# Kernel optimization log

Hardware: AMD Instinct MI355X
Metric: run time of the kernel (lower is better)

The kernel has to match this reference:

```python
import jax, jax.numpy as jnp
import numpy as np

B, S, D, H, F = 8, 1024, 768, 12, 3072
DH = D // H
C_QUAD = 5.0
LN_EPS = 1e-5


def layer_norm(x, g, b):
    mu = jnp.mean(x, axis=-1, keepdims=True)
    var = jnp.mean(jnp.square(x - mu), axis=-1, keepdims=True)
    return (x - mu) * jax.lax.rsqrt(var + LN_EPS) * g + b


def setup_inputs() -> dict:
    key = jax.random.key(0)
    ks = jax.random.split(key, 8)
    s_in = 1.0 / np.sqrt(D)
    s_ff = 1.0 / np.sqrt(F)
    return {
        "x": jax.random.normal(ks[0], (B, S, D), jnp.float32),
        "wqkv": jax.random.normal(ks[1], (D, 3 * D), jnp.float32) * s_in,
        "bqkv": jnp.zeros((3 * D,), jnp.float32),
        "wo": jax.random.normal(ks[2], (D, D), jnp.float32) * s_in,
        "bo": jnp.zeros((D,), jnp.float32),
        "ln1_g": jnp.ones((D,), jnp.float32),
        "ln1_b": jnp.zeros((D,), jnp.float32),
        "w1": jax.random.normal(ks[3], (D, F), jnp.float32) * s_in,
        "b1": jnp.zeros((F,), jnp.float32),
        "w2": jax.random.normal(ks[4], (F, D), jnp.float32) * s_ff,
        "b2": jnp.zeros((D,), jnp.float32),
        "ln2_g": jnp.ones((D,), jnp.float32),
        "ln2_b": jnp.zeros((D,), jnp.float32),
    }


def quad2(scores):
    # Quad2 custom 'softmax': (s + c)^2 normalized by row sum
    s2 = jnp.square(scores + C_QUAD)
    return s2 / jnp.sum(s2, axis=-1, keepdims=True)


def reference(x, wqkv, bqkv, wo, bo, ln1_g, ln1_b, w1, b1, w2, b2, ln2_g, ln2_b):
    # --- pre-norm multi-head attention with Quad2 score normalization ---
    h = layer_norm(x, ln1_g, ln1_b)
    qkv = h @ wqkv + bqkv                              # [B,S,3D]
    q, k, v = jnp.split(qkv, 3, axis=-1)
    q = q.reshape(B, S, H, DH).transpose(0, 2, 1, 3)   # [B,H,S,Dh]
    k = k.reshape(B, S, H, DH).transpose(0, 2, 1, 3)
    v = v.reshape(B, S, H, DH).transpose(0, 2, 1, 3)
    scale = 1.0 / np.sqrt(DH)
    scores = jnp.einsum("bhqd,bhkd->bhqk", q, k) * scale
    attn = quad2(scores)                               # [B,H,S,S]
    ctx = jnp.einsum("bhqk,bhkd->bhqd", attn, v)
    ctx = ctx.transpose(0, 2, 1, 3).reshape(B, S, D)
    x = x + ctx @ wo + bo
    # --- pre-norm FFN ---
    h = layer_norm(x, ln2_g, ln2_b)
    h = jax.nn.gelu(h @ w1 + b1)
    x = x + h @ w2 + b2
    return x
```

## Files before the change

### kernel.cpp

```cpp
#include <hip/hip_runtime.h>
#include <hip/hip_bf16.h>

constexpr int B_ = 8;
constexpr int S_ = 1024;
constexpr int D_ = 768;
constexpr int H_ = 12;
constexpr int F_ = 3072;
constexpr int DH_ = 64;
constexpr int M_ = B_ * S_;
constexpr int PSZ = B_ * S_ * D_;

typedef __bf16 bf16x8 __attribute__((ext_vector_type(8)));
typedef float f32x4 __attribute__((ext_vector_type(4)));
typedef short s16x8 __attribute__((ext_vector_type(8)));
typedef short s16x4 __attribute__((ext_vector_type(4)));

__device__ __forceinline__ void gload_lds16(const __bf16* g, __bf16* l) {
    __builtin_amdgcn_global_load_lds(
        (const __attribute__((address_space(1))) void*)g,
        (__attribute__((address_space(3))) void*)l,
        16, 0, 0);
}

__device__ __forceinline__ float fast_gelu(float x) {
    float x3 = x * x * x;
    float z = 0.7978845608028654f * x + 0.035677408136300125f * x3;
    float e = __builtin_amdgcn_exp2f(-2.8853900817779268f * z);
    return x * __builtin_amdgcn_rcpf(1.0f + e);
}

__global__ __launch_bounds__(256) void transpose_cvt(const float* __restrict__ in,
                                                     __bf16* __restrict__ out,
                                                     int K, int N) {
    __shared__ float t[32][33];
    int tx = threadIdx.x, ty = threadIdx.y;
    int n0 = blockIdx.x * 32, k0 = blockIdx.y * 32;
#pragma unroll
    for (int i = 0; i < 4; ++i)
        t[ty + i * 8][tx] = in[(size_t)(k0 + ty + i * 8) * N + n0 + tx];
    __syncthreads();
#pragma unroll
    for (int i = 0; i < 4; ++i)
        out[(size_t)(n0 + ty + i * 8) * K + k0 + tx] = (__bf16)t[tx][ty + i * 8];
}

__global__ __launch_bounds__(256) void ln_kernel(const float* __restrict__ x,
                                                 const float* __restrict__ g,
                                                 const float* __restrict__ bb,
                                                 __bf16* __restrict__ out) {
    int row = blockIdx.x;
    const float* xr = x + (size_t)row * D_;
    int tid = threadIdx.x;
    float v[3];
    float s = 0.f, s2 = 0.f;
#pragma unroll
    for (int j = 0; j < 3; ++j) {
        v[j] = xr[tid + j * 256];
        s += v[j];
        s2 += v[j] * v[j];
    }
#pragma unroll
    for (int o = 32; o >= 1; o >>= 1) {
        s += __shfl_xor(s, o, 64);
        s2 += __shfl_xor(s2, o, 64);
    }
    __shared__ float red[8];
    int wid = tid >> 6, lane = tid & 63;
    if (lane == 0) { red[wid] = s; red[4 + wid] = s2; }
    __syncthreads();
    s = red[0] + red[1] + red[2] + red[3];
    s2 = red[4] + red[5] + red[6] + red[7];
    float mu = s * (1.0f / D_);
    float var = s2 * (1.0f / D_) - mu * mu;
    float rs = rsqrtf(var + 1e-5f);
    __bf16* orow = out + (size_t)row * D_;
#pragma unroll
    for (int j = 0; j < 3; ++j) {
        int i = tid + j * 256;
        orow[i] = (__bf16)((v[j] - mu) * rs * g[i] + bb[i]);
    }
}

template <int EPI>
__device__ __forceinline__ void gemm4_body(const __bf16* __restrict__ A,
                                           const __bf16* __restrict__ Bt,
                                           const float* __restrict__ bias,
                                           const float* __restrict__ res,
                                           float* __restrict__ outf,
                                           __bf16* __restrict__ outb,
                                           int M, int N, int K) {
    __shared__ __bf16 lds[2][16384];

    const int tid = threadIdx.x;
    const int lane = tid & 63, wid = tid >> 6;
    const int wm = wid >> 1, wn = wid & 1;
    const int gx = gridDim.x;
    const int nwg = gx * gridDim.y;
    int flat = blockIdx.y * gx + blockIdx.x;
    flat = (flat & 7) * (nwg >> 3) + (flat >> 3);
    const int bm = (flat / gx) * 128, bn = (flat % gx) * 128;
    const int l15 = lane & 15, l4 = lane >> 4;
    f32x4 acc[4][4] = {};

    const int r8 = tid >> 3;
    const int swc = ((tid & 7) ^ (r8 & 7)) * 8;
    const __bf16* ga = A + (size_t)(bm + r8) * K + swc;
    const __bf16* gb = Bt + (size_t)(bn + r8) * K + swc;
    const int NT = K / 64;

    auto stage = [&](int t, int s) {
        const int kt = t * 64;
        __bf16* base = &lds[s][0] + tid * 8;
#pragma unroll
        for (int j = 0; j < 4; ++j)
            gload_lds16(ga + kt + (size_t)j * 32 * K, base + j * 2048);
#pragma unroll
        for (int j = 0; j < 4; ++j)
            gload_lds16(gb + kt + (size_t)j * 32 * K, base + 8192 + j * 2048);
    };

    stage(0, 0);
    for (int t = 0; t < NT; ++t) {
        if (t + 1 < NT) {
            stage(t + 1, (t + 1) & 1);
            asm volatile("s_waitcnt vmcnt(8)" ::: "memory");
        } else {
            asm volatile("s_waitcnt vmcnt(0)" ::: "memory");
        }
        asm volatile("s_barrier" ::: "memory");

        const __bf16* sA = &lds[t & 1][0];
        const __bf16* sB = sA + 8192;
        const int swr = (l15 & 7) * 8;
        bf16x8 a[4][2], b[4][2];
#pragma unroll
        for (int mf = 0; mf < 4; ++mf) {
            int row = wm * 64 + mf * 16 + l15;
#pragma unroll
            for (int ks = 0; ks < 2; ++ks)
                a[mf][ks] = *(const bf16x8*)&sA[row * 64 + ((ks * 32 + l4 * 8) ^ swr)];
        }
#pragma unroll
        for (int nf = 0; nf < 4; ++nf) {
            int row = wn * 64 + nf * 16 + l15;
#pragma unroll
            for (int ks = 0; ks < 2; ++ks)
                b[nf][ks] = *(const bf16x8*)&sB[row * 64 + ((ks * 32 + l4 * 8) ^ swr)];
        }
        asm volatile("s_waitcnt lgkmcnt(0)" ::: "memory");
        asm volatile("s_barrier" ::: "memory");
        __builtin_amdgcn_sched_barrier(0);

        __builtin_amdgcn_s_setprio(1);
#pragma unroll
        for (int ks = 0; ks < 2; ++ks)
#pragma unroll
            for (int mf = 0; mf < 4; ++mf)
#pragma unroll
                for (int nf = 0; nf < 4; ++nf)
                    acc[mf][nf] = __builtin_amdgcn_mfma_f32_16x16x32_bf16(
                        a[mf][ks], b[nf][ks], acc[mf][nf], 0, 0, 0);
        __builtin_amdgcn_s_setprio(0);
    }

    if constexpr (EPI == 0) {
#pragma unroll
        for (int nf = 0; nf < 4; ++nf) {
            int n = bn + wn * 64 + nf * 16 + l15;
            int part = n / 768;
            int n7 = n - part * 768;
            float bv = bias[n];
            size_t obase = (size_t)part * PSZ + (size_t)(n7 >> 6) * (S_ * DH_) + (n7 & 63);
#pragma unroll
            for (int mf = 0; mf < 4; ++mf) {
                int m0 = bm + wm * 64 + mf * 16 + l4 * 4;
                size_t rb = obase + (size_t)(m0 >> 10) * ((size_t)H_ * S_ * DH_) +
                            (size_t)(m0 & 1023) * DH_;
#pragma unroll
                for (int r = 0; r < 4; ++r)
                    outb[rb + (size_t)r * DH_] = (__bf16)(acc[mf][nf][r] + bv);
            }
        }
    } else {
#pragma unroll
        for (int mf = 0; mf < 4; ++mf) {
#pragma unroll
            for (int nf = 0; nf < 4; ++nf) {
#pragma unroll
                for (int r = 0; r < 4; ++r) {
                    int m = bm + wm * 64 + mf * 16 + l4 * 4 + r;
                    int n = bn + wn * 64 + nf * 16 + l15;
                    float val = acc[mf][nf][r] + bias[n];
                    if constexpr (EPI == 1) {
                        outf[(size_t)m * N + n] = val + res[(size_t)m * N + n];
                    } else {
                        outb[(size_t)m * N + n] = (__bf16)fast_gelu(val);
                    }
                }
            }
        }
    }
}

template <int EPI>
__device__ __forceinline__ void gemmk_body(const __bf16* __restrict__ A,
                                           const __bf16* __restrict__ Bt,
                                           const float* __restrict__ bias,
                                           const float* __restrict__ res,
                                           float* __restrict__ outf,
                                           __bf16* __restrict__ outb,
                                           int M, int N, int K) {
    __shared__ __bf16 lds[2][16384];

    const int tid = threadIdx.x;
    const int lane = tid & 63, wid = tid >> 6;
    const int wm = wid >> 2, wn = wid & 3;
    const int gx = gridDim.x;
    const int nwg = gx * gridDim.y;
    int flat = blockIdx.y * gx + blockIdx.x;
    flat = (flat & 7) * (nwg >> 3) + (flat >> 3);
    const int bm = (flat / gx) * 128, bn = (flat % gx) * 128;
    const int l15 = lane & 15, l4 = lane >> 4;
    f32x4 acc[4][2] = {};

    const int r8 = tid >> 3;
    const int swc = ((tid & 7) ^ (r8 & 7)) * 8;
    const __bf16* ga = A + (size_t)(bm + r8) * K + swc;
    const __bf16* gb = Bt + (size_t)(bn + r8) * K + swc;
    const int NT = K / 64;

    auto stage = [&](int t, int s) {
        const int kt = t * 64;
        __bf16* base = &lds[s][0] + tid * 8;
        gload_lds16(ga + kt, base);
        gload_lds16(ga + kt + (size_t)64 * K, base + 4096);
        gload_lds16(gb + kt, base + 8192);
        gload_lds16(gb + kt + (size_t)64 * K, base + 12288);
    };

    stage(0, 0);
    for (int t = 0; t < NT; ++t) {
        if (t + 1 < NT) {
            stage(t + 1, (t + 1) & 1);
            asm volatile("s_waitcnt vmcnt(4)" ::: "memory");
        } else {
            asm volatile("s_waitcnt vmcnt(0)" ::: "memory");
        }
        asm volatile("s_barrier" ::: "memory");

        const __bf16* sA = &lds[t & 1][0];
        const __bf16* sB = sA + 8192;
        const int swr = (l15 & 7) * 8;
        bf16x8 a[4][2], b[2][2];
#pragma unroll
        for (int mf = 0; mf < 4; ++mf) {
            int row = wm * 64 + mf * 16 + l15;
#pragma unroll
            for (int ks = 0; ks < 2; ++ks)
                a[mf][ks] = *(const bf16x8*)&sA[row * 64 + ((ks * 32 + l4 * 8) ^ swr)];
        }
#pragma unroll
        for (int nf = 0; nf < 2; ++nf) {
            int row = wn * 32 + nf * 16 + l15;
#pragma unroll
            for (int ks = 0; ks < 2; ++ks)
                b[nf][ks] = *(const bf16x8*)&sB[row * 64 + ((ks * 32 + l4 * 8) ^ swr)];
        }
        asm volatile("s_waitcnt lgkmcnt(0)" ::: "memory");
        asm volatile("s_barrier" ::: "memory");
        __builtin_amdgcn_sched_barrier(0);

        __builtin_amdgcn_s_setprio(1);
#pragma unroll
        for (int ks = 0; ks < 2; ++ks)
#pragma unroll
            for (int mf = 0; mf < 4; ++mf)
#pragma unroll
                for (int nf = 0; nf < 2; ++nf)
                    acc[mf][nf] = __builtin_amdgcn_mfma_f32_16x16x32_bf16(
                        a[mf][ks], b[nf][ks], acc[mf][nf], 0, 0, 0);
        __builtin_amdgcn_s_setprio(0);
    }

#pragma unroll
    for (int mf = 0; mf < 4; ++mf) {
#pragma unroll
        for (int nf = 0; nf < 2; ++nf) {
#pragma unroll
            for (int r = 0; r < 4; ++r) {
                int m = bm + wm * 64 + mf * 16 + l4 * 4 + r;
                int n = bn + wn * 32 + nf * 16 + l15;
                float val = acc[mf][nf][r] + bias[n];
                if constexpr (EPI == 1) {
                    outf[(size_t)m * N + n] = val + res[(size_t)m * N + n];
                } else {
                    outb[(size_t)m * N + n] = (__bf16)fast_gelu(val);
                }
            }
        }
    }
    (void)outf;
}

__global__ __launch_bounds__(256) void g_qkv(const __bf16* A, const __bf16* Bt,
                                             const float* bias, __bf16* outb) {
    gemm4_body<0>(A, Bt, bias, nullptr, nullptr, outb, M_, 3 * D_, D_);
}
__global__ __launch_bounds__(256) void g_proj(const __bf16* A, const __bf16* Bt,
                                              const float* bias, const float* res,
                                              float* outf) {
    gemm4_body<1>(A, Bt, bias, res, outf, nullptr, M_, D_, D_);
}
__global__ __launch_bounds__(512) void g_ffn1(const __bf16* A, const __bf16* Bt,
                                              const float* bias, __bf16* outb) {
    gemmk_body<2>(A, Bt, bias, nullptr, nullptr, outb, M_, F_, D_);
}
__global__ __launch_bounds__(512) void g_ffn2(const __bf16* A, const __bf16* Bt,
                                              const float* bias, const float* res,
                                              float* outf) {
    gemmk_body<1>(A, Bt, bias, res, outf, nullptr, M_, D_, F_);
}

__global__ __launch_bounds__(256) void attn_kernel(const __bf16* __restrict__ qg,
                                                   const __bf16* __restrict__ kg,
                                                   const __bf16* __restrict__ vg,
                                                   __bf16* __restrict__ ctx) {
    __shared__ __bf16 Ks[64][72];
    __shared__ __bf16 Vt[64][72];
    __shared__ __bf16 Pw[4][32][72];
    __shared__ float den_l[4][32];
    int tid = threadIdx.x, lane = tid & 63, wid = tid >> 6;
    int l15 = lane & 15, l4 = lane >> 4;
    int idx = blockIdx.x;
    int xcd = idx & 7;
    int c = idx >> 3;
    int bh = xcd * 12 + (c >> 3);
    int qt = c & 7;
    int q0 = qt * 128;
    const __bf16* qbase = qg + (size_t)bh * S_ * DH_;
    const __bf16* kbase = kg + (size_t)bh * S_ * DH_;
    const __bf16* vbase = vg + (size_t)bh * S_ * DH_;

    int wq0 = q0 + wid * 32;
    bf16x8 qf[2][2];
#pragma unroll
    for (int qi = 0; qi < 2; ++qi)
#pragma unroll
        for (int ks = 0; ks < 2; ++ks)
            qf[qi][ks] = *(const bf16x8*)(qbase + (size_t)(wq0 + qi * 16 + l15) * DH_ +
                                          ks * 32 + l4 * 8);

    f32x4 oacc[2][4] = {};
    float den[2] = {0.f, 0.f};
    const float scale = 0.125f;

    for (int k0 = 0; k0 < S_; k0 += 64) {
        {
            int key = tid >> 2, dc = (tid & 3) * 16;
            *(s16x8*)&Ks[key][dc] =
                *(const s16x8*)(kbase + (size_t)(k0 + key) * DH_ + dc);
            *(s16x8*)&Ks[key][dc + 8] =
                *(const s16x8*)(kbase + (size_t)(k0 + key) * DH_ + dc + 8);
            int vkey = tid & 63, dg = (tid >> 6) * 16;
            s16x8 v0 = *(const s16x8*)(vbase + (size_t)(k0 + vkey) * DH_ + dg);
            s16x8 v1 = *(const s16x8*)(vbase + (size_t)(k0 + vkey) * DH_ + dg + 8);
#pragma unroll
            for (int e = 0; e < 8; ++e) {
                Vt[dg + e][vkey] = ((const __bf16*)&v0)[e];
                Vt[dg + 8 + e][vkey] = ((const __bf16*)&v1)[e];
            }
        }
        __syncthreads();

        bf16x8 kf[4][2];
#pragma unroll
        for (int kfi = 0; kfi < 4; ++kfi)
#pragma unroll
            for (int ks = 0; ks < 2; ++ks)
                kf[kfi][ks] = *(const bf16x8*)&Ks[kfi * 16 + l15][ks * 32 + l4 * 8];

#pragma unroll
        for (int qi = 0; qi < 2; ++qi) {
#pragma unroll
            for (int kfi = 0; kfi < 4; ++kfi) {
                f32x4 sa = {};
                sa = __builtin_amdgcn_mfma_f32_16x16x32_bf16(kf[kfi][0], qf[qi][0], sa, 0, 0, 0);
                sa = __builtin_amdgcn_mfma_f32_16x16x32_bf16(kf[kfi][1], qf[qi][1], sa, 0, 0, 0);
                __bf16 pk[4];
#pragma unroll
                for (int r = 0; r < 4; ++r) {
                    float p = sa[r] * scale + 5.0f;
                    p = p * p;
                    den[qi] += p;
                    pk[r] = (__bf16)p;
                }
                *(s16x4*)&Pw[wid][qi * 16 + l15][kfi * 16 + l4 * 4] =
                    *(const s16x4*)pk;
            }
        }

#pragma unroll
        for (int mf = 0; mf < 2; ++mf) {
#pragma unroll
            for (int ks = 0; ks < 2; ++ks) {
                bf16x8 pa = *(const bf16x8*)&Pw[wid][mf * 16 + l15][ks * 32 + l4 * 8];
#pragma unroll
                for (int nf = 0; nf < 4; ++nf) {
                    bf16x8 vb = *(const bf16x8*)&Vt[nf * 16 + l15][ks * 32 + l4 * 8];
                    oacc[mf][nf] = __builtin_amdgcn_mfma_f32_16x16x32_bf16(
                        pa, vb, oacc[mf][nf], 0, 0, 0);
                }
            }
        }
        __syncthreads();
    }

#pragma unroll
    for (int qi = 0; qi < 2; ++qi) {
        den[qi] += __shfl_xor(den[qi], 16, 64);
        den[qi] += __shfl_xor(den[qi], 32, 64);
    }
    if (lane < 16) {
        den_l[wid][lane] = den[0];
        den_l[wid][16 + lane] = den[1];
    }
    __syncthreads();

    int b_ = bh / H_, h_ = bh - b_ * H_;
#pragma unroll
    for (int mf = 0; mf < 2; ++mf)
#pragma unroll
        for (int nf = 0; nf < 4; ++nf) {
#pragma unroll
            for (int r = 0; r < 4; ++r) {
                int qrow = mf * 16 + l4 * 4 + r;
                int dcol = nf * 16 + l15;
                float val = oacc[mf][nf][r] *
                            __builtin_amdgcn_rcpf(den_l[wid][qrow]);
                int sI = q0 + wid * 32 + qrow;
                ctx[((size_t)b_ * S_ + sI) * D_ + h_ * DH_ + dcol] = (__bf16)val;
            }
        }
}

extern "C" void kernel_launch(void* const* d_in, const int* in_sizes, int n_in,
                              void* d_out, int out_size, void* d_ws, size_t ws_size,
                              hipStream_t stream) {
    const float* x    = (const float*)d_in[0];
    const float* wqkv = (const float*)d_in[1];
    const float* bqkv = (const float*)d_in[2];
    const float* wo   = (const float*)d_in[3];
    const float* bo   = (const float*)d_in[4];
    const float* ln1g = (const float*)d_in[5];
    const float* ln1b = (const float*)d_in[6];
    const float* w1   = (const float*)d_in[7];
    const float* b1   = (const float*)d_in[8];
    const float* w2   = (const float*)d_in[9];
    const float* b2   = (const float*)d_in[10];
    const float* ln2g = (const float*)d_in[11];
    const float* ln2b = (const float*)d_in[12];
    float* out = (float*)d_out;

    char* ws = (char*)d_ws;
    size_t off = 0;
    auto alloc = [&](size_t bytes) {
        void* p = ws + off;
        off += (bytes + 255) & ~(size_t)255;
        return p;
    };
    __bf16* wqkvT = (__bf16*)alloc((size_t)(3 * D_) * D_ * 2);
    __bf16* woT   = (__bf16*)alloc((size_t)D_ * D_ * 2);
    __bf16* w1T   = (__bf16*)alloc((size_t)F_ * D_ * 2);
    __bf16* w2T   = (__bf16*)alloc((size_t)D_ * F_ * 2);
    float*  X2    = (float*)alloc((size_t)M_ * D_ * 4);
    __bf16* Hb    = (__bf16*)alloc((size_t)M_ * D_ * 2);
    __bf16* Q3    = (__bf16*)alloc((size_t)4 * PSZ * 2);
    __bf16* Kb = Q3 + (size_t)PSZ;
    __bf16* Vb = Q3 + (size_t)2 * PSZ;
    __bf16* Cx = Q3 + (size_t)3 * PSZ;

    transpose_cvt<<<dim3((3 * D_) / 32, D_ / 32), dim3(32, 8), 0, stream>>>(wqkv, wqkvT, D_, 3 * D_);
    transpose_cvt<<<dim3(D_ / 32, D_ / 32), dim3(32, 8), 0, stream>>>(wo, woT, D_, D_);
    transpose_cvt<<<dim3(F_ / 32, D_ / 32), dim3(32, 8), 0, stream>>>(w1, w1T, D_, F_);
    transpose_cvt<<<dim3(D_ / 32, F_ / 32), dim3(32, 8), 0, stream>>>(w2, w2T, F_, D_);

    ln_kernel<<<M_, 256, 0, stream>>>(x, ln1g, ln1b, Hb);
    g_qkv<<<dim3((3 * D_) / 128, M_ / 128), 256, 0, stream>>>(Hb, wqkvT, bqkv, Q3);
    attn_kernel<<<B_ * H_ * (S_ / 128), 256, 0, stream>>>(Q3, Kb, Vb, Cx);
    g_proj<<<dim3(D_ / 128, M_ / 128), 256, 0, stream>>>(Cx, woT, bo, x, X2);
    ln_kernel<<<M_, 256, 0, stream>>>(X2, ln2g, ln2b, Hb);
    g_ffn1<<<dim3(F_ / 128, M_ / 128), 512, 0, stream>>>(Hb, w1T, b1, Q3);
    g_ffn2<<<dim3(D_ / 128, M_ / 128), 512, 0, stream>>>(Q3, w2T, b2, X2, out);
    (void)in_sizes; (void)n_in; (void)out_size; (void)ws_size;
}
```

Baseline: 226.1 us.

## Replace 512-thread FFN GEMM with 256-thread triple-buffered K32 kernel, simplify attention mapping

```diff
diff --git a/kernel.cpp b/kernel.cpp
--- a/kernel.cpp
+++ b/kernel.cpp
@@ -203,68 +203,62 @@
 }
 
 template <int EPI>
-__device__ __forceinline__ void gemmk_body(const __bf16* __restrict__ A,
-                                           const __bf16* __restrict__ Bt,
-                                           const float* __restrict__ bias,
-                                           const float* __restrict__ res,
-                                           float* __restrict__ outf,
-                                           __bf16* __restrict__ outb,
-                                           int M, int N, int K) {
-    __shared__ __bf16 lds[2][16384];
+__device__ __forceinline__ void gemm32_body(const __bf16* __restrict__ A,
+                                            const __bf16* __restrict__ Bt,
+                                            const float* __restrict__ bias,
+                                            const float* __restrict__ res,
+                                            float* __restrict__ outf,
+                                            __bf16* __restrict__ outb,
+                                            int M, int N, int K) {
+    __shared__ __bf16 lds[3][8192];
 
     const int tid = threadIdx.x;
     const int lane = tid & 63, wid = tid >> 6;
-    const int wm = wid >> 2, wn = wid & 3;
+    const int wm = wid >> 1, wn = wid & 1;
     const int gx = gridDim.x;
     const int nwg = gx * gridDim.y;
     int flat = blockIdx.y * gx + blockIdx.x;
     flat = (flat & 7) * (nwg >> 3) + (flat >> 3);
     const int bm = (flat / gx) * 128, bn = (flat % gx) * 128;
     const int l15 = lane & 15, l4 = lane >> 4;
-    f32x4 acc[4][2] = {};
-
-    const int r8 = tid >> 3;
-    const int swc = ((tid & 7) ^ (r8 & 7)) * 8;
+    f32x4 acc[4][4] = {};
+
+    const int r8 = tid >> 2;
+    const int cg = tid & 3;
+    const int swc = (cg ^ (r8 & 3)) * 8;
     const __bf16* ga = A + (size_t)(bm + r8) * K + swc;
     const __bf16* gb = Bt + (size_t)(bn + r8) * K + swc;
-    const int NT = K / 64;
+    const int NT = K / 32;
 
     auto stage = [&](int t, int s) {
-        const int kt = t * 64;
+        const int kt = t * 32;
         __bf16* base = &lds[s][0] + tid * 8;
         gload_lds16(ga + kt, base);
-        gload_lds16(ga + kt + (size_t)64 * K, base + 4096);
-        gload_lds16(gb + kt, base + 8192);
-        gload_lds16(gb + kt + (size_t)64 * K, base + 12288);
+        gload_lds16(ga + kt + (size_t)64 * K, base + 2048);
+        gload_lds16(gb + kt, base + 4096);
+        gload_lds16(gb + kt + (size_t)64 * K, base + 6144);
     };
 
     stage(0, 0);
+    stage(1, 1);
     for (int t = 0; t < NT; ++t) {
-        if (t + 1 < NT) {
-            stage(t + 1, (t + 1) & 1);
-            asm volatile("s_waitcnt vmcnt(4)" ::: "memory");
-        } else {
-            asm volatile("s_waitcnt vmcnt(0)" ::: "memory");
-        }
+        stage(t + 2 < NT ? t + 2 : NT - 1, (t + 2) % 3);
+        asm volatile("s_waitcnt vmcnt(8)" ::: "memory");
         asm volatile("s_barrier" ::: "memory");
 
-        const __bf16* sA = &lds[t & 1][0];
-        const __bf16* sB = sA + 8192;
-        const int swr = (l15 & 7) * 8;
-        bf16x8 a[4][2], b[2][2];
+        const __bf16* sA = &lds[t % 3][0];
+        const __bf16* sB = sA + 4096;
+        const int swr = (l15 & 3) * 8;
+        bf16x8 a[4], b[4];
 #pragma unroll
         for (int mf = 0; mf < 4; ++mf) {
             int row = wm * 64 + mf * 16 + l15;
-#pragma unroll
-            for (int ks = 0; ks < 2; ++ks)
-                a[mf][ks] = *(const bf16x8*)&sA[row * 64 + ((ks * 32 + l4 * 8) ^ swr)];
-        }
-#pragma unroll
-        for (int nf = 0; nf < 2; ++nf) {
-            int row = wn * 32 + nf * 16 + l15;
-#pragma unroll
-            for (int ks = 0; ks < 2; ++ks)
-                b[nf][ks] = *(const bf16x8*)&sB[row * 64 + ((ks * 32 + l4 * 8) ^ swr)];
+            a[mf] = *(const bf16x8*)&sA[row * 32 + ((l4 * 8) ^ swr)];
+        }
+#pragma unroll
+        for (int nf = 0; nf < 4; ++nf) {
+            int row = wn * 64 + nf * 16 + l15;
+            b[nf] = *(const bf16x8*)&sB[row * 32 + ((l4 * 8) ^ swr)];
         }
         asm volatile("s_waitcnt lgkmcnt(0)" ::: "memory");
         asm volatile("s_barrier" ::: "memory");
@@ -272,24 +266,22 @@
 
         __builtin_amdgcn_s_setprio(1);
 #pragma unroll
-        for (int ks = 0; ks < 2; ++ks)
-#pragma unroll
-            for (int mf = 0; mf < 4; ++mf)
-#pragma unroll
-                for (int nf = 0; nf < 2; ++nf)
-                    acc[mf][nf] = __builtin_amdgcn_mfma_f32_16x16x32_bf16(
-                        a[mf][ks], b[nf][ks], acc[mf][nf], 0, 0, 0);
+        for (int mf = 0; mf < 4; ++mf)
+#pragma unroll
+            for (int nf = 0; nf < 4; ++nf)
+                acc[mf][nf] = __builtin_amdgcn_mfma_f32_16x16x32_bf16(
+                    a[mf], b[nf], acc[mf][nf], 0, 0, 0);
         __builtin_amdgcn_s_setprio(0);
     }
 
 #pragma unroll
     for (int mf = 0; mf < 4; ++mf) {
 #pragma unroll
-        for (int nf = 0; nf < 2; ++nf) {
+        for (int nf = 0; nf < 4; ++nf) {
 #pragma unroll
             for (int r = 0; r < 4; ++r) {
                 int m = bm + wm * 64 + mf * 16 + l4 * 4 + r;
-                int n = bn + wn * 32 + nf * 16 + l15;
+                int n = bn + wn * 64 + nf * 16 + l15;
                 float val = acc[mf][nf][r] + bias[n];
                 if constexpr (EPI == 1) {
                     outf[(size_t)m * N + n] = val + res[(size_t)m * N + n];
@@ -311,14 +303,14 @@
                                               float* outf) {
     gemm4_body<1>(A, Bt, bias, res, outf, nullptr, M_, D_, D_);
 }
-__global__ __launch_bounds__(512) void g_ffn1(const __bf16* A, const __bf16* Bt,
+__global__ __launch_bounds__(256) void g_ffn1(const __bf16* A, const __bf16* Bt,
                                               const float* bias, __bf16* outb) {
-    gemmk_body<2>(A, Bt, bias, nullptr, nullptr, outb, M_, F_, D_);
-}
-__global__ __launch_bounds__(512) void g_ffn2(const __bf16* A, const __bf16* Bt,
+    gemm32_body<2>(A, Bt, bias, nullptr, nullptr, outb, M_, F_, D_);
+}
+__global__ __launch_bounds__(256) void g_ffn2(const __bf16* A, const __bf16* Bt,
                                               const float* bias, const float* res,
                                               float* outf) {
-    gemmk_body<1>(A, Bt, bias, res, outf, nullptr, M_, D_, F_);
+    gemm4_body<1>(A, Bt, bias, res, outf, nullptr, M_, D_, F_);
 }
 
 __global__ __launch_bounds__(256) void attn_kernel(const __bf16* __restrict__ qg,
@@ -331,11 +323,7 @@
     __shared__ float den_l[4][32];
     int tid = threadIdx.x, lane = tid & 63, wid = tid >> 6;
     int l15 = lane & 15, l4 = lane >> 4;
-    int idx = blockIdx.x;
-    int xcd = idx & 7;
-    int c = idx >> 3;
-    int bh = xcd * 12 + (c >> 3);
-    int qt = c & 7;
+    int bh = blockIdx.x >> 3, qt = blockIdx.x & 7;
     int q0 = qt * 128;
     const __bf16* qbase = qg + (size_t)bh * S_ * DH_;
     const __bf16* kbase = kg + (size_t)bh * S_ * DH_;
@@ -489,7 +477,7 @@
     attn_kernel<<<B_ * H_ * (S_ / 128), 256, 0, stream>>>(Q3, Kb, Vb, Cx);
     g_proj<<<dim3(D_ / 128, M_ / 128), 256, 0, stream>>>(Cx, woT, bo, x, X2);
     ln_kernel<<<M_, 256, 0, stream>>>(X2, ln2g, ln2b, Hb);
-    g_ffn1<<<dim3(F_ / 128, M_ / 128), 512, 0, stream>>>(Hb, w1T, b1, Q3);
-    g_ffn2<<<dim3(D_ / 128, M_ / 128), 512, 0, stream>>>(Q3, w2T, b2, X2, out);
+    g_ffn1<<<dim3(F_ / 128, M_ / 128), 256, 0, stream>>>(Hb, w1T, b1, Q3);
+    g_ffn2<<<dim3(D_ / 128, M_ / 128), 256, 0, stream>>>(Q3, w2T, b2, X2, out);
     (void)in_sizes; (void)n_in; (void)out_size; (void)ws_size;
 }
```

New measurement: 246.3 us. +9.0%, slower.
